# Kernel tuning notes

Hardware: AMD Instinct MI355X
Metric: run time of the kernel (lower is better)

Reference implementation:

```python
import jax, jax.numpy as jnp
import numpy as np

B, S, D, H, HD = 4, 2048, 1024, 16, 64
R, L = 4, 256
MASKED_BIAS = -10000.0


def setup_inputs() -> dict:
    key = jax.random.key(0)
    ks = jax.random.split(key, 8)
    w = 0.02  # GPT-2 style init scale keeps softmax logits sane
    return {
        "hidden_states": jax.random.normal(ks[0], (B, S, D), jnp.float32),
        "latent": jax.random.normal(ks[1], (B, L), jnp.float32),
        "c_attn_w": jax.random.normal(ks[2], (D, 3 * D), jnp.float32) * w,
        "c_attn_b": jnp.zeros((3 * D,), jnp.float32),
        "c_proj_w": jax.random.normal(ks[3], (D, D), jnp.float32) * w,
        "c_proj_b": jnp.zeros((D,), jnp.float32),
        "text_w": jax.random.normal(ks[4], (R, D + 1, D), jnp.float32) * w,
        "text_b": jnp.zeros((R, D), jnp.float32),
        "lat_w": jax.random.normal(ks[5], (R, L + 1, D), jnp.float32) * w,
        "lat_b": jnp.zeros((R, D), jnp.float32),
    }


def _lmf(v, latent, text_w, text_b, lat_w, lat_b):
    # append bias-1 column, apply rank-R linears, sum over rank, outer-fuse
    b, s, _ = v.shape
    v1 = jnp.concatenate([v, jnp.ones((b, s, 1), v.dtype)], axis=-1)          # [B,S,D+1]
    l1 = jnp.concatenate([latent, jnp.ones((b, 1), latent.dtype)], axis=-1)   # [B,L+1]
    text_fusion = jnp.einsum("bsi,rio->bso", v1, text_w) + text_b.sum(0)      # [B,S,D]
    latent_fusion = jnp.einsum("bi,rio->bo", l1, lat_w) + lat_b.sum(0)        # [B,D]
    return text_fusion * latent_fusion[:, None, :]


def reference(hidden_states, latent, c_attn_w, c_attn_b, c_proj_w, c_proj_b,
              text_w, text_b, lat_w, lat_b):
    qkv = hidden_states @ c_attn_w + c_attn_b                # [B,S,3D] (Conv1D)
    q, k, v = jnp.split(qkv, 3, axis=-1)
    v = _lmf(v, latent, text_w, text_b, lat_w, lat_b)        # LMF on value stream

    def split_heads(t):
        return t.reshape(B, S, H, HD).transpose(0, 2, 1, 3)  # [B,H,S,HD]

    q, k, v = split_heads(q), split_heads(k), split_heads(v)
    scores = jnp.einsum("bhqd,bhkd->bhqk", q, k) / jnp.asarray(HD, q.dtype) ** 0.5
    causal = jnp.tril(jnp.ones((S, S), bool))                # use_causal_mask=True
    scores = jnp.where(causal, scores, jnp.asarray(MASKED_BIAS, scores.dtype))
    probs = jax.nn.softmax(scores, axis=-1)                  # attn_pdrop=0 (eval)
    attn = jnp.einsum("bhqk,bhkd->bhqd", probs, v)
    attn = attn.transpose(0, 2, 1, 3).reshape(B, S, D)       # merge heads
    return attn @ c_proj_w + c_proj_b                        # resid_pdrop=0 (eval)
```

## Files before the change

### kernel.cpp

```cpp
#include <hip/hip_runtime.h>
#include <hip/hip_bf16.h>

typedef __bf16 bf16;
typedef __bf16 bf16x8 __attribute__((ext_vector_type(8)));
typedef float f32x4 __attribute__((ext_vector_type(4)));
typedef unsigned short u16;
typedef unsigned int u32;

__device__ __forceinline__ u16 f2bf_bits(float f) {
    union { float f; u32 u; } v;
    v.f = f;
    u32 r = v.u + 0x7FFFu + ((v.u >> 16) & 1u);
    return (u16)(r >> 16);
}

__device__ __forceinline__ void gload_lds16(const void* g, void* l) {
    __builtin_amdgcn_global_load_lds((const __attribute__((address_space(1))) void*)g,
                                     (__attribute__((address_space(3))) void*)l, 16, 0, 0);
}


__global__ __launch_bounds__(256) void cvt_bf16_kernel(const float* __restrict__ in,
                                                       u32* __restrict__ out, int n4) {
    int i = blockIdx.x * 256 + threadIdx.x;
    if (i < n4) {
        float4 v = reinterpret_cast<const float4*>(in)[i];
        u32 lo = (u32)f2bf_bits(v.x) | ((u32)f2bf_bits(v.y) << 16);
        u32 hi = (u32)f2bf_bits(v.z) | ((u32)f2bf_bits(v.w) << 16);
        reinterpret_cast<uint2*>(out)[i] = make_uint2(lo, hi);
    }
}

__global__ __launch_bounds__(256) void transpose_sum_bf16(const float* __restrict__ in,
                                                          u16* __restrict__ out,
                                                          int K, int N, int R, long slab) {
    __shared__ float tile[32][33];
    int x = threadIdx.x & 31, ty = threadIdx.x >> 5;
    int k0 = blockIdx.y * 32, n0 = blockIdx.x * 32;
    for (int yy = ty; yy < 32; yy += 8) {
        float s = 0.f;
        for (int r = 0; r < R; ++r)
            s += in[(size_t)r * slab + (size_t)(k0 + yy) * N + n0 + x];
        tile[yy][x] = s;
    }
    __syncthreads();
    for (int yy = ty; yy < 32; yy += 8)
        out[(size_t)(n0 + yy) * K + k0 + x] = f2bf_bits(tile[x][yy]);
}

__global__ __launch_bounds__(256) void btfull_kernel(const float* __restrict__ tw,
                                                     const float* __restrict__ tb,
                                                     float* __restrict__ bt) {
    int o = blockIdx.x * 256 + threadIdx.x;
    float s = 0.f;
    for (int r = 0; r < 4; ++r)
        s += tw[(size_t)r * 1025 * 1024 + (size_t)1024 * 1024 + o] + tb[r * 1024 + o];
    bt[o] = s;
}

__global__ __launch_bounds__(256) void latfuse_kernel(const float* __restrict__ latent,
                                                      const float* __restrict__ lw,
                                                      const float* __restrict__ lb,
                                                      float* __restrict__ lf) {
    int o = blockIdx.x * 256 + threadIdx.x;
    int b = blockIdx.y;
    float s = 0.f;
    for (int r = 0; r < 4; ++r) {
        const float* w = lw + (size_t)r * 257 * 1024;
        float acc = 0.f;
        for (int i = 0; i < 256; ++i) acc += latent[b * 256 + i] * w[(size_t)i * 1024 + o];
        acc += w[(size_t)256 * 1024 + o];
        acc += lb[r * 1024 + o];
        s += acc;
    }
    lf[b * 1024 + o] = s;
}

template <int EPI>
__global__ __launch_bounds__(256) void gemm_bt(const bf16* __restrict__ A, int lda,
                                               const bf16* __restrict__ BT, int ldb,
                                               void* __restrict__ Cout, int ldc, int K,
                                               const float* __restrict__ bias,
                                               const float* __restrict__ scale) {
    __shared__ __align__(16) char As[16384];
    __shared__ __align__(16) char Bs[16384];
    const int tid = threadIdx.x;
    const int w = tid >> 6, l = tid & 63;

    const int nwgx = gridDim.x;
    const int nwg = nwgx * gridDim.y;
    const int wgid = blockIdx.y * nwgx + blockIdx.x;
    const int swz = (wgid & 7) * (nwg >> 3) + (wgid >> 3);
    const int m0 = (swz / nwgx) * 128, n0 = (swz % nwgx) * 128;
    const int wr = (w >> 1) * 64, wc = (w & 1) * 64;

    f32x4 acc[4][4] = {};
    const int kIters = K >> 6;

    const int srow = tid >> 3;
    const int scol = (tid & 7) * 8;
    const size_t aBase = (size_t)(m0 + srow) * lda + scol;
    const size_t bBase = (size_t)(n0 + srow) * ldb + scol;
    char* AsW = As + w * 1024;
    char* BsW = Bs + w * 1024;

    for (int kt = 0; kt < kIters; ++kt) {
        const int kk = kt << 6;
#pragma unroll
        for (int i = 0; i < 4; ++i) {
            gload_lds16(A + aBase + (size_t)(i * 32) * lda + kk, AsW + i * 4096);
            gload_lds16(BT + bBase + (size_t)(i * 32) * ldb + kk, BsW + i * 4096);
        }
        __syncthreads();
#pragma unroll
        for (int dc = 0; dc < 2; ++dc) {
            bf16x8 af[4], bfr[4];
#pragma unroll
            for (int m = 0; m < 4; ++m) {
                int off = (wr + m * 16 + (l & 15)) * 128 + dc * 64 + (l >> 4) * 16;
                af[m] = *reinterpret_cast<const bf16x8*>(As + off);
            }
#pragma unroll
            for (int n = 0; n < 4; ++n) {
                int off = (wc + n * 16 + (l & 15)) * 128 + dc * 64 + (l >> 4) * 16;
                bfr[n] = *reinterpret_cast<const bf16x8*>(Bs + off);
            }
#pragma unroll
            for (int m = 0; m < 4; ++m)
#pragma unroll
                for (int n = 0; n < 4; ++n)
                    acc[m][n] = __builtin_amdgcn_mfma_f32_16x16x32_bf16(af[m], bfr[n], acc[m][n], 0, 0, 0);
        }
        __syncthreads();
    }

#pragma unroll
    for (int m = 0; m < 4; ++m) {
#pragma unroll
        for (int n = 0; n < 4; ++n) {
#pragma unroll
            for (int r = 0; r < 4; ++r) {
                int grow = m0 + wr + m * 16 + (l >> 4) * 4 + r;
                int gcol = n0 + wc + n * 16 + (l & 15);
                float v = acc[m][n][r];
                if (EPI == 0 || EPI == 1) v += bias[gcol];
                if (EPI == 2) {
                    v += bias[grow];
                    v *= scale[((gcol >> 11) << 10) | grow];
                }
                if (EPI == 1)
                    reinterpret_cast<float*>(Cout)[(size_t)grow * ldc + gcol] = v;
                else
                    reinterpret_cast<u16*>(Cout)[(size_t)grow * ldc + gcol] = f2bf_bits(v);
            }
        }
    }
}

__global__ __launch_bounds__(256) void attn_kernel(const bf16* __restrict__ qkv,
                                                   const bf16* __restrict__ vfT,
                                                   u16* __restrict__ out) {
    __shared__ __align__(16) char Kl[2][8192];
    __shared__ __align__(16) char Vt[2][8192];
    __shared__ __align__(16) char Pl[4][4096];
    const int tid = threadIdx.x, w = tid >> 6, l = tid & 63;
    const int bh = blockIdx.y, b = bh >> 4, h = bh & 15;
    const float SCL = 0.125f * 1.44269504089f;
    char* Pw = Pl[w];

    const int srowL = (l >> 3);
    const int cs = ((l & 7) ^ srowL) * 8;

    for (int ph = 0; ph < 2; ++ph) {
        const int qt = ph ? (15 - blockIdx.x) : blockIdx.x;
        const int q0 = qt * 128;
        const size_t rowQ = (size_t)(b * 2048 + q0 + w * 32);

        bf16x8 qfr[2][2];
#pragma unroll
        for (int qf = 0; qf < 2; ++qf)
#pragma unroll
            for (int dc = 0; dc < 2; ++dc)
                qfr[qf][dc] = *reinterpret_cast<const bf16x8*>(
                    qkv + (rowQ + qf * 16 + (l & 15)) * 3072 + h * 64 + dc * 32 + (l >> 4) * 8);

        f32x4 oacc[2][4] = {};
        float mrun[2] = {-1e30f, -1e30f};
        float lrun[2] = {0.f, 0.f};
        const int nt = (q0 + 128) >> 6;
        const int qmaxw = q0 + w * 32 + 31;

        auto stage = [&](int t, int buf) {
            const size_t kvb = (size_t)(b * 2048 + t * 64);
#pragma unroll
            for (int i = 0; i < 2; ++i) {
                int r = w * 8 + i * 32 + srowL;
                gload_lds16(qkv + (kvb + r) * 3072 + 1024 + h * 64 + cs,
                            Kl[buf] + w * 1024 + i * 4096);
                gload_lds16(vfT + (size_t)(h * 64 + r) * 8192 + kvb + cs,
                            Vt[buf] + w * 1024 + i * 4096);
            }
        };

        __syncthreads();
        stage(0, 0);
        int cur = 0;
        for (int t = 0; t < nt; ++t) {
            __syncthreads();
            if (t + 1 < nt) stage(t + 1, cur ^ 1);
            const int kv0 = t * 64;
            if (kv0 <= qmaxw) {
                const char* Kb = Kl[cur];
                const char* Vb = Vt[cur];
                f32x4 sacc[4][2] = {};
#pragma unroll
                for (int dc = 0; dc < 2; ++dc) {
#pragma unroll
                    for (int kf = 0; kf < 4; ++kf) {
                        int row = kf * 16 + (l & 15);
                        int off = (row * 128 + dc * 64 + (l >> 4) * 16) ^ ((row & 7) << 4);
                        bf16x8 kfr = *reinterpret_cast<const bf16x8*>(Kb + off);
#pragma unroll
                        for (int qf = 0; qf < 2; ++qf)
                            sacc[kf][qf] = __builtin_amdgcn_mfma_f32_16x16x32_bf16(
                                kfr, qfr[qf][dc], sacc[kf][qf], 0, 0, 0);
                    }
                }
                const bool needMask = (kv0 + 63) > (q0 + w * 32);
#pragma unroll
                for (int qf = 0; qf < 2; ++qf) {
                    int qg = q0 + w * 32 + qf * 16 + (l & 15);
                    float sv[4][4];
                    float tmax = -1e30f;
#pragma unroll
                    for (int kf = 0; kf < 4; ++kf)
#pragma unroll
                        for (int r = 0; r < 4; ++r) {
                            float s = sacc[kf][qf][r] * SCL;
                            if (needMask) {
                                int kvg = kv0 + kf * 16 + (l >> 4) * 4 + r;
                                if (kvg > qg) s = -1e30f;
                            }
                            sv[kf][r] = s;
                            tmax = fmaxf(tmax, s);
                        }
                    tmax = fmaxf(tmax, __shfl_xor(tmax, 16));
                    tmax = fmaxf(tmax, __shfl_xor(tmax, 32));
                    if (!__all(tmax <= mrun[qf] + 8.f)) {
                        float mnew = fmaxf(mrun[qf], tmax);
                        float alpha = exp2f(mrun[qf] - mnew);
                        mrun[qf] = mnew;
                        lrun[qf] *= alpha;
#pragma unroll
                        for (int r = 0; r < 4; ++r) {
                            float al = __shfl(alpha, (l >> 4) * 4 + r);
#pragma unroll
                            for (int hf = 0; hf < 4; ++hf) oacc[qf][hf][r] *= al;
                        }
                    }
                    const float m = mrun[qf];
                    float rsum = 0.f;
                    int qlocal = qf * 16 + (l & 15);
#pragma unroll
                    for (int kf = 0; kf < 4; ++kf) {
                        float p0 = exp2f(sv[kf][0] - m), p1 = exp2f(sv[kf][1] - m);
                        float p2 = exp2f(sv[kf][2] - m), p3 = exp2f(sv[kf][3] - m);
                        rsum += (p0 + p1) + (p2 + p3);
                        uint2 pk;
                        pk.x = (u32)f2bf_bits(p0) | ((u32)f2bf_bits(p1) << 16);
                        pk.y = (u32)f2bf_bits(p2) | ((u32)f2bf_bits(p3) << 16);
                        int off = (qlocal * 128 + kf * 32 + (l >> 4) * 8) ^ ((qlocal & 7) << 4);
                        *reinterpret_cast<uint2*>(Pw + off) = pk;
                    }
                    rsum += __shfl_xor(rsum, 16);
                    rsum += __shfl_xor(rsum, 32);
                    lrun[qf] += rsum;
                }
#pragma unroll
                for (int kc = 0; kc < 2; ++kc) {
                    bf16x8 pa[2];
#pragma unroll
                    for (int qf = 0; qf < 2; ++qf) {
                        int qlocal = qf * 16 + (l & 15);
                        int off = (qlocal * 128 + kc * 64 + (l >> 4) * 16) ^ ((qlocal & 7) << 4);
                        pa[qf] = *reinterpret_cast<const bf16x8*>(Pw + off);
                    }
#pragma unroll
                    for (int hf = 0; hf < 4; ++hf) {
                        int hd = hf * 16 + (l & 15);
                        int off = (hd * 128 + kc * 64 + (l >> 4) * 16) ^ ((hd & 7) << 4);
                        bf16x8 vb = *reinterpret_cast<const bf16x8*>(Vb + off);
#pragma unroll
                        for (int qf = 0; qf < 2; ++qf)
                            oacc[qf][hf] = __builtin_amdgcn_mfma_f32_16x16x32_bf16(
                                pa[qf], vb, oacc[qf][hf], 0, 0, 0);
                    }
                }
            }
            cur ^= 1;
        }

#pragma unroll
        for (int qf = 0; qf < 2; ++qf) {
#pragma unroll
            for (int r = 0; r < 4; ++r) {
                float linv = 1.0f / __shfl(lrun[qf], (l >> 4) * 4 + r);
                size_t grow = rowQ + qf * 16 + (l >> 4) * 4 + r;
#pragma unroll
                for (int hf = 0; hf < 4; ++hf)
                    out[grow * 1024 + h * 64 + hf * 16 + (l & 15)] =
                        f2bf_bits(oacc[qf][hf][r] * linv);
            }
        }
    }
}


extern "C" void kernel_launch(void* const* d_in, const int* in_sizes, int n_in,
                              void* d_out, int out_size, void* d_ws, size_t ws_size,
                              hipStream_t stream) {
    const float* hs     = (const float*)d_in[0];
    const float* latent = (const float*)d_in[1];
    const float* attnw  = (const float*)d_in[2];
    const float* attnb  = (const float*)d_in[3];
    const float* projw  = (const float*)d_in[4];
    const float* projb  = (const float*)d_in[5];
    const float* textw  = (const float*)d_in[6];
    const float* textb  = (const float*)d_in[7];
    const float* latw   = (const float*)d_in[8];
    const float* latb   = (const float*)d_in[9];

    char* ws = (char*)d_ws;
    size_t off = 0;
    auto alloc = [&](size_t bytes) {
        char* p = ws + off;
        off += (bytes + 255) & ~(size_t)255;
        return p;
    };
    u16* qkv    = (u16*)alloc((size_t)8192 * 3072 * 2);
    u16* hsbf   = (u16*)alloc((size_t)8192 * 1024 * 2);
    u16* vfT    = (u16*)alloc((size_t)1024 * 8192 * 2);
    u16* attnWT = (u16*)alloc((size_t)3072 * 1024 * 2);
    u16* projWT = (u16*)alloc((size_t)1024 * 1024 * 2);
    u16* WtT    = (u16*)alloc((size_t)1024 * 1024 * 2);
    float* btf  = (float*)alloc(1024 * 4);
    float* lf   = (float*)alloc(4 * 1024 * 4);

    cvt_bf16_kernel<<<8192, 256, 0, stream>>>(hs, (u32*)hsbf, 8192 * 1024 / 4);
    transpose_sum_bf16<<<dim3(96, 32), 256, 0, stream>>>(attnw, attnWT, 1024, 3072, 1, 0);
    transpose_sum_bf16<<<dim3(32, 32), 256, 0, stream>>>(projw, projWT, 1024, 1024, 1, 0);
    transpose_sum_bf16<<<dim3(32, 32), 256, 0, stream>>>(textw, WtT, 1024, 1024, 4, (long)1025 * 1024);
    btfull_kernel<<<4, 256, 0, stream>>>(textw, textb, btf);
    latfuse_kernel<<<dim3(4, 4), 256, 0, stream>>>(latent, latw, latb, lf);

    gemm_bt<0><<<dim3(24, 64), 256, 0, stream>>>(
        (const bf16*)hsbf, 1024, (const bf16*)attnWT, 1024, qkv, 3072, 1024, attnb, nullptr);
    gemm_bt<2><<<dim3(64, 8), 256, 0, stream>>>(
        (const bf16*)WtT, 1024, (const bf16*)qkv + 2048, 3072, vfT, 8192, 1024, btf, lf);
    attn_kernel<<<dim3(8, 64), 256, 0, stream>>>((const bf16*)qkv, (const bf16*)vfT, hsbf);
    gemm_bt<1><<<dim3(8, 64), 256, 0, stream>>>(
        (const bf16*)hsbf, 1024, (const bf16*)projWT, 1024, d_out, 1024, 1024, projb, nullptr);
}
```

Baseline: 453.9 us.

## Keep attention probabilities in registers via lane shuffles, prescale Q in GEMM epilogue

The softmax probabilities are no longer written to and read back from a per-wave LDS buffer. Instead they are packed to bf16 and rearranged across lanes with xor shuffles straight into the MFMA A-operand layout. The 1/sqrt(d)*log2e scale is moved into the QKV GEMM epilogue for the Q columns, removing a multiply per score. The attention kernel also drops 16KB of LDS and declares launch bounds of 4 blocks per SM to raise occupancy, which may force register spills.

```diff
diff --git a/kernel.cpp b/kernel.cpp
--- a/kernel.cpp
+++ b/kernel.cpp
@@ -12,6 +12,13 @@
     v.f = f;
     u32 r = v.u + 0x7FFFu + ((v.u >> 16) & 1u);
     return (u16)(r >> 16);
+}
+
+__device__ __forceinline__ u32 pack_bf2(float a, float b) {
+    union { __bf16 h[2]; u32 u; } v;
+    v.h[0] = (__bf16)a;
+    v.h[1] = (__bf16)b;
+    return v.u;
 }
 
 __device__ __forceinline__ void gload_lds16(const void* g, void* l) {
@@ -134,6 +141,7 @@
         __syncthreads();
     }
 
+    const bool qtile = (EPI == 3) && (n0 < 1024);
 #pragma unroll
     for (int m = 0; m < 4; ++m) {
 #pragma unroll
@@ -143,7 +151,8 @@
                 int grow = m0 + wr + m * 16 + (l >> 4) * 4 + r;
                 int gcol = n0 + wc + n * 16 + (l & 15);
                 float v = acc[m][n][r];
-                if (EPI == 0 || EPI == 1) v += bias[gcol];
+                if (EPI == 1 || EPI == 3) v += bias[gcol];
+                if (EPI == 3 && qtile) v *= 0.18033688011f;
                 if (EPI == 2) {
                     v += bias[grow];
                     v *= scale[((gcol >> 11) << 10) | grow];
@@ -157,16 +166,13 @@
     }
 }
 
-__global__ __launch_bounds__(256) void attn_kernel(const bf16* __restrict__ qkv,
-                                                   const bf16* __restrict__ vfT,
-                                                   u16* __restrict__ out) {
+__global__ __launch_bounds__(256, 4) void attn_kernel(const bf16* __restrict__ qkv,
+                                                      const bf16* __restrict__ vfT,
+                                                      u16* __restrict__ out) {
     __shared__ __align__(16) char Kl[2][8192];
     __shared__ __align__(16) char Vt[2][8192];
-    __shared__ __align__(16) char Pl[4][4096];
     const int tid = threadIdx.x, w = tid >> 6, l = tid & 63;
     const int bh = blockIdx.y, b = bh >> 4, h = bh & 15;
-    const float SCL = 0.125f * 1.44269504089f;
-    char* Pw = Pl[w];
 
     const int srowL = (l >> 3);
     const int cs = ((l & 7) ^ srowL) * 8;
@@ -227,21 +233,22 @@
                     }
                 }
                 const bool needMask = (kv0 + 63) > (q0 + w * 32);
+                bf16x8 pa[2][2];
 #pragma unroll
                 for (int qf = 0; qf < 2; ++qf) {
                     int qg = q0 + w * 32 + qf * 16 + (l & 15);
-                    float sv[4][4];
+                    float p[4][4];
                     float tmax = -1e30f;
 #pragma unroll
                     for (int kf = 0; kf < 4; ++kf)
 #pragma unroll
                         for (int r = 0; r < 4; ++r) {
-                            float s = sacc[kf][qf][r] * SCL;
+                            float s = sacc[kf][qf][r];
                             if (needMask) {
                                 int kvg = kv0 + kf * 16 + (l >> 4) * 4 + r;
                                 if (kvg > qg) s = -1e30f;
                             }
-                            sv[kf][r] = s;
+                            p[kf][r] = s;
                             tmax = fmaxf(tmax, s);
                         }
                     tmax = fmaxf(tmax, __shfl_xor(tmax, 16));
@@ -260,31 +267,45 @@
                     }
                     const float m = mrun[qf];
                     float rsum = 0.f;
-                    int qlocal = qf * 16 + (l & 15);
 #pragma unroll
                     for (int kf = 0; kf < 4; ++kf) {
-                        float p0 = exp2f(sv[kf][0] - m), p1 = exp2f(sv[kf][1] - m);
-                        float p2 = exp2f(sv[kf][2] - m), p3 = exp2f(sv[kf][3] - m);
+                        float p0 = exp2f(p[kf][0] - m), p1 = exp2f(p[kf][1] - m);
+                        float p2 = exp2f(p[kf][2] - m), p3 = exp2f(p[kf][3] - m);
+                        p[kf][0] = p0; p[kf][1] = p1; p[kf][2] = p2; p[kf][3] = p3;
                         rsum += (p0 + p1) + (p2 + p3);
-                        uint2 pk;
-                        pk.x = (u32)f2bf_bits(p0) | ((u32)f2bf_bits(p1) << 16);
-                        pk.y = (u32)f2bf_bits(p2) | ((u32)f2bf_bits(p3) << 16);
-                        int off = (qlocal * 128 + kf * 32 + (l >> 4) * 8) ^ ((qlocal & 7) << 4);
-                        *reinterpret_cast<uint2*>(Pw + off) = pk;
                     }
                     rsum += __shfl_xor(rsum, 16);
                     rsum += __shfl_xor(rsum, 32);
                     lrun[qf] += rsum;
+                    u32 c[4][2];
+#pragma unroll
+                    for (int kf = 0; kf < 4; ++kf) {
+                        c[kf][0] = pack_bf2(p[kf][0], p[kf][1]);
+                        c[kf][1] = pack_bf2(p[kf][2], p[kf][3]);
+                    }
+#pragma unroll
+                    for (int kc = 0; kc < 2; ++kc) {
+                        u32 wlo[2], whi[2];
+#pragma unroll
+                        for (int hh = 0; hh < 2; ++hh) {
+                            u32 oe = c[2 * kc][hh], oo = c[2 * kc + 1][hh];
+                            u32 xoe = (u32)__shfl_xor((int)oe, 32);
+                            u32 xoo = (u32)__shfl_xor((int)oo, 32);
+                            u32 P1 = (l & 32) ? xoo : oe;
+                            u32 P2 = (l & 32) ? oo : xoe;
+                            u32 z = (l & 16) ? P1 : P2;
+                            u32 xz = (u32)__shfl_xor((int)z, 16);
+                            wlo[hh] = (l & 16) ? xz : P1;
+                            whi[hh] = (l & 16) ? P2 : xz;
+                        }
+                        union { u32 u[4]; bf16x8 v; } pv;
+                        pv.u[0] = wlo[0]; pv.u[1] = wlo[1];
+                        pv.u[2] = whi[0]; pv.u[3] = whi[1];
+                        pa[qf][kc] = pv.v;
+                    }
                 }
 #pragma unroll
                 for (int kc = 0; kc < 2; ++kc) {
-                    bf16x8 pa[2];
-#pragma unroll
-                    for (int qf = 0; qf < 2; ++qf) {
-                        int qlocal = qf * 16 + (l & 15);
-                        int off = (qlocal * 128 + kc * 64 + (l >> 4) * 16) ^ ((qlocal & 7) << 4);
-                        pa[qf] = *reinterpret_cast<const bf16x8*>(Pw + off);
-                    }
 #pragma unroll
                     for (int hf = 0; hf < 4; ++hf) {
                         int hd = hf * 16 + (l & 15);
@@ -293,7 +314,7 @@
 #pragma unroll
                         for (int qf = 0; qf < 2; ++qf)
                             oacc[qf][hf] = __builtin_amdgcn_mfma_f32_16x16x32_bf16(
-                                pa[qf], vb, oacc[qf][hf], 0, 0, 0);
+                                pa[qf][kc], vb, oacc[qf][hf], 0, 0, 0);
                     }
                 }
             }
@@ -353,7 +374,7 @@
     btfull_kernel<<<4, 256, 0, stream>>>(textw, textb, btf);
     latfuse_kernel<<<dim3(4, 4), 256, 0, stream>>>(latent, latw, latb, lf);
 
-    gemm_bt<0><<<dim3(24, 64), 256, 0, stream>>>(
+    gemm_bt<3><<<dim3(24, 64), 256, 0, stream>>>(
         (const bf16*)hsbf, 1024, (const bf16*)attnWT, 1024, qkv, 3072, 1024, attnb, nullptr);
     gemm_bt<2><<<dim3(64, 8), 256, 0, stream>>>(
         (const bf16*)WtT, 1024, (const bf16*)qkv + 2048, 3072, vfT, 8192, 1024, btf, lf);
```

Measured after the change: 506.1 us. 11.5% more time.
